# Kernel optimization log

Hardware: AMD Instinct MI355X
Metric: run time of the kernel (lower is better)

Reference implementation:

```python
import jax, jax.numpy as jnp
import numpy as np

HQ, HKV, HD = 32, 8, 64
ROPE_BASE = 10000.0


def _rope_cos_sin(L):
    # torchtune-style interleaved RoPE cache
    theta = 1.0 / (ROPE_BASE ** (jnp.arange(0, HD, 2, dtype=jnp.float32) / HD))  # [HD/2]
    ang = jnp.arange(L, dtype=jnp.float32)[:, None] * theta[None, :]             # [L, HD/2]
    return jnp.cos(ang)[None, :, None, :], jnp.sin(ang)[None, :, None, :]        # [1,L,1,HD/2]


def _apply_rope(t, cos, sin):
    # t: [B, L, H, HD]; pairs are interleaved along last dim
    x = t.reshape(t.shape[:-1] + (HD // 2, 2))
    x0, x1 = x[..., 0], x[..., 1]
    out = jnp.stack([x0 * cos - x1 * sin, x1 * cos + x0 * sin], axis=-1)
    return out.reshape(t.shape)


def setup_inputs() -> dict:
    key = jax.random.key(0)
    k1, k2, k3 = jax.random.split(key, 3)
    B, L, D = 2, 2048, 2048
    x = jax.random.normal(k1, (B, L, D), dtype=jnp.float32)
    w_qkv = jax.random.normal(k2, ((HQ + 2 * HKV) * HD, D), dtype=jnp.float32) * 0.02
    w_o = jax.random.normal(k3, (D, D), dtype=jnp.float32) * 0.02
    return {"x": x, "w_qkv": w_qkv, "w_o": w_o}


def reference(x, w_qkv, w_o):
    B, L, D = x.shape
    G = HQ // HKV  # q heads per kv head
    qkv = x @ w_qkv.T  # [B, L, (HQ+2*HKV)*HD]
    q = qkv[..., : HQ * HD].reshape(B, L, HQ, HD)
    k = qkv[..., HQ * HD : (HQ + HKV) * HD].reshape(B, L, HKV, HD)
    v = qkv[..., (HQ + HKV) * HD :].reshape(B, L, HKV, HD)

    cos, sin = _rope_cos_sin(L)
    q = _apply_rope(q, cos, sin)
    k = _apply_rope(k, cos, sin)

    # GQA: q head h attends with kv head h // G
    q = q.transpose(0, 2, 1, 3).reshape(B, HKV, G, L, HD)
    k = k.transpose(0, 2, 1, 3)  # [B, HKV, L, HD]
    v = v.transpose(0, 2, 1, 3)

    scale = 1.0 / jnp.sqrt(jnp.float32(HD))
    scores = jnp.einsum('bhgqd,bhkd->bhgqk', q, k) * scale  # [B,HKV,G,L,L]
    causal = jnp.tril(jnp.ones((L, L), dtype=bool))
    scores = jnp.where(causal, scores, jnp.finfo(scores.dtype).min)
    attn = jax.nn.softmax(scores, axis=-1)
    y = jnp.einsum('bhgqk,bhkd->bhgqd', attn, v)            # [B,HKV,G,L,HD]
    y = y.reshape(B, HQ, L, HD).transpose(0, 2, 1, 3).reshape(B, L, D)
    return y @ w_o.T
```

## Files before the change

### kernel.cpp

```cpp
#include <hip/hip_runtime.h>

typedef __attribute__((ext_vector_type(8))) short bf16x8;
typedef __attribute__((ext_vector_type(4))) float f32x4;

__device__ __forceinline__ float bf2f(unsigned short u) {
  unsigned int x = ((unsigned int)u) << 16;
  float f; __builtin_memcpy(&f, &x, 4); return f;
}
__device__ __forceinline__ unsigned short f2bf(float f) {
  unsigned int x; __builtin_memcpy(&x, &f, 4);
  unsigned int lsb = (x >> 16) & 1u;
  x += 0x7fffu + lsb;
  return (unsigned short)(x >> 16);
}
__device__ __forceinline__ unsigned short f2bf_trunc(float f) {
  unsigned int x; __builtin_memcpy(&x, &f, 4);
  return (unsigned short)(x >> 16);
}
__device__ __forceinline__ float exp2_raw(float x) {
  float r;
  asm("v_exp_f32 %0, %1" : "=v"(r) : "v"(x));
  return r;
}
__device__ __forceinline__ void gload16(const unsigned short* g, unsigned short* l) {
  __builtin_amdgcn_global_load_lds(
      (const __attribute__((address_space(1))) unsigned int*)g,
      (__attribute__((address_space(3))) unsigned int*)l, 16, 0, 0);
}

__global__ __launch_bounds__(256) void cvt3(const float* __restrict__ x,
                                            const float* __restrict__ wq,
                                            const float* __restrict__ wo,
                                            unsigned short* __restrict__ xb,
                                            unsigned short* __restrict__ wqb,
                                            unsigned short* __restrict__ wob) {
  const int N0 = 1048576, N1 = 786432, N2 = 524288;
  for (int i = blockIdx.x * 256 + threadIdx.x; i < N0 + N1 + N2;
       i += (int)(gridDim.x * 256)) {
    const float* in; unsigned short* out; int j;
    if (i < N0)            { in = x;  out = xb;  j = i; }
    else if (i < N0 + N1)  { in = wq; out = wqb; j = i - N0; }
    else                   { in = wo; out = wob; j = i - N0 - N1; }
    const float4* p = (const float4*)(in + (size_t)j * 8);
    float4 a = p[0], b = p[1];
    union { bf16x8 v; unsigned short u[8]; } o;
    o.u[0] = f2bf(a.x); o.u[1] = f2bf(a.y); o.u[2] = f2bf(a.z); o.u[3] = f2bf(a.w);
    o.u[4] = f2bf(b.x); o.u[5] = f2bf(b.y); o.u[6] = f2bf(b.z); o.u[7] = f2bf(b.w);
    *(bf16x8*)(out + (size_t)j * 8) = o.v;
  }
}

template <int F32OUT>
__global__ __launch_bounds__(256) void gemm_bt(const unsigned short* __restrict__ A,
                                               const unsigned short* __restrict__ B,
                                               void* __restrict__ Cp, int N) {
  __shared__ unsigned short sA[128 * 32];
  __shared__ unsigned short sB[128 * 32];
  const int t = threadIdx.x;
  const int lane = t & 63, w = t >> 6;
  const int wm = w >> 1, wn = w & 1;
  const int l16 = lane & 15, hi = lane >> 4;
  const int m0 = blockIdx.y * 128, n0 = blockIdx.x * 128;

  f32x4 zero = {0.f, 0.f, 0.f, 0.f};
  f32x4 acc[4][4];
#pragma unroll
  for (int mi = 0; mi < 4; ++mi)
#pragma unroll
    for (int ni = 0; ni < 4; ++ni) acc[mi][ni] = zero;

  const int srow = t >> 2;
  const int scol = (t & 3) * 8;
  const unsigned short* gA0 = A + (size_t)(m0 + srow) * 2048 + scol;
  const unsigned short* gB0 = B + (size_t)(n0 + srow) * 2048 + scol;

  int offA[4], offB[4];
#pragma unroll
  for (int i = 0; i < 4; ++i) {
    offA[i] = (wm * 64 + i * 16 + l16) * 32 + hi * 8;
    offB[i] = (wn * 64 + i * 16 + l16) * 32 + hi * 8;
  }

  for (int k0 = 0; k0 < 2048; k0 += 32) {
    __syncthreads();
    gload16(gA0 + k0, &sA[t * 8]);
    gload16(gA0 + (size_t)64 * 2048 + k0, &sA[2048 + t * 8]);
    gload16(gB0 + k0, &sB[t * 8]);
    gload16(gB0 + (size_t)64 * 2048 + k0, &sB[2048 + t * 8]);
    __syncthreads();
    bf16x8 af[4], bfr[4];
#pragma unroll
    for (int i = 0; i < 4; ++i) af[i] = *(const bf16x8*)&sA[offA[i]];
#pragma unroll
    for (int i = 0; i < 4; ++i) bfr[i] = *(const bf16x8*)&sB[offB[i]];
#pragma unroll
    for (int mi = 0; mi < 4; ++mi)
#pragma unroll
      for (int ni = 0; ni < 4; ++ni)
        acc[mi][ni] = __builtin_amdgcn_mfma_f32_16x16x32_bf16(af[mi], bfr[ni], acc[mi][ni], 0, 0, 0);
  }

  const int rowb = m0 + wm * 64 + hi * 4;
  const int colb = n0 + wn * 64 + l16;
#pragma unroll
  for (int mi = 0; mi < 4; ++mi)
#pragma unroll
    for (int ni = 0; ni < 4; ++ni)
#pragma unroll
      for (int r = 0; r < 4; ++r) {
        size_t idx = (size_t)(rowb + mi * 16 + r) * N + colb + ni * 16;
        if (F32OUT) ((float*)Cp)[idx] = acc[mi][ni][r];
        else        ((unsigned short*)Cp)[idx] = f2bf(acc[mi][ni][r]);
      }
}

__global__ __launch_bounds__(256) void prep(const unsigned short* __restrict__ qkv,
                                            unsigned short* __restrict__ q,
                                            unsigned short* __restrict__ k,
                                            unsigned short* __restrict__ vt) {
  __shared__ unsigned short sT[64 * 72];
  const int bid = blockIdx.x;
  if (bid < 640) {
    int tid = bid * 256 + threadIdx.x;
    int l = tid & 2047;
    int rest = tid >> 11;
    int b = rest & 1;
    int h = rest >> 1;
    const unsigned short* src = qkv + (size_t)(b * 2048 + l) * 3072 + h * 64;
    union { uint4 v[8]; unsigned short u[64]; } buf;
#pragma unroll
    for (int i = 0; i < 8; ++i) buf.v[i] = ((const uint4*)src)[i];
    const float sc = (h < 32) ? 0.125f * 1.44269504088896f : 1.0f;
#pragma unroll
    for (int j = 0; j < 32; ++j) {
      float fr = exp2f(-(float)j * 0.41524101186092033f);
      float ang = (float)l * fr;
      float sn, cs;
      sincosf(ang, &sn, &cs);
      float x0 = bf2f(buf.u[2 * j]), x1 = bf2f(buf.u[2 * j + 1]);
      float y0 = (x0 * cs - x1 * sn) * sc;
      float y1 = (x1 * cs + x0 * sn) * sc;
      buf.u[2 * j] = f2bf(y0);
      buf.u[2 * j + 1] = f2bf(y1);
    }
    unsigned short* dst = (h < 32) ? (q + ((size_t)(b * 32 + h) * 2048 + l) * 64)
                                   : (k + ((size_t)(b * 8 + h - 32) * 2048 + l) * 64);
#pragma unroll
    for (int i = 0; i < 8; ++i) ((uint4*)dst)[i] = buf.v[i];
  } else {
    const int bid2 = bid - 640;
    const int xb = bid2 & 31, bh = bid2 >> 5;
    const int t = threadIdx.x;
    const int b = bh >> 3, h = bh & 7;
    const int l0 = xb * 64;
    const int c = t & 7, i0 = t >> 3;
#pragma unroll
    for (int pp = 0; pp < 2; ++pp) {
      int i = i0 + pp * 32;
      const unsigned short* src =
          qkv + (size_t)(b * 2048 + l0 + i) * 3072 + 2560 + h * 64 + c * 8;
      union { bf16x8 v; unsigned short u[8]; } x;
      x.v = *(const bf16x8*)src;
#pragma unroll
      for (int e = 0; e < 8; ++e) sT[(c * 8 + e) * 72 + i] = x.u[e];
    }
    __syncthreads();
    const int d = t >> 2, ic = (t & 3) * 16;
    unsigned short* dst = vt + ((size_t)(b * 8 + h) * 64 + d) * 2048 + l0 + ic;
    *(bf16x8*)dst = *(const bf16x8*)&sT[d * 72 + ic];
    *(bf16x8*)(dst + 8) = *(const bf16x8*)&sT[d * 72 + ic + 8];
  }
}

__global__ __launch_bounds__(256) void attn(const unsigned short* __restrict__ Q,
                                            const unsigned short* __restrict__ K,
                                            const unsigned short* __restrict__ VT,
                                            unsigned short* __restrict__ Y) {
  __shared__ unsigned short sK[128 * 64];
  __shared__ unsigned short sV[64 * 128];
  __shared__ unsigned short sP[4][32 * 136];
  const int t = threadIdx.x, lane = t & 63, w = t >> 6;
  const int l16 = lane & 15, hi = lane >> 4;
  const int pi = blockIdx.y;
  const int bx = blockIdx.x;
  const int head = ((bx & 7) << 3) | (bx >> 3);
  const int b = head >> 5, hq = head & 31, hkv = hq >> 2;
  const unsigned short* kp = K + (size_t)(b * 8 + hkv) * 2048 * 64;
  const unsigned short* vp = VT + (size_t)(b * 8 + hkv) * 64 * 2048;
  unsigned short* sPw = sP[w];
  f32x4 zero = {0.f, 0.f, 0.f, 0.f};

#pragma unroll
  for (int phase = 0; phase < 2; ++phase) {
    const int qb = phase ? (15 - pi) : pi;
    const int q0 = qb * 128 + w * 32;
    const unsigned short* qp = Q + ((size_t)(b * 32 + hq) * 2048 + q0) * 64;

    bf16x8 qf[2][2];
#pragma unroll
    for (int mi = 0; mi < 2; ++mi)
#pragma unroll
      for (int ks = 0; ks < 2; ++ks)
        qf[mi][ks] = *(const bf16x8*)(qp + (size_t)(mi * 16 + l16) * 64 + ks * 32 + hi * 8);

    f32x4 o[2][4];
    float lsum[2][4];
#pragma unroll
    for (int mi = 0; mi < 2; ++mi) {
#pragma unroll
      for (int ni = 0; ni < 4; ++ni) o[mi][ni] = zero;
#pragma unroll
      for (int r = 0; r < 4; ++r) lsum[mi][r] = 0.f;
    }

    const int nt = qb + 1;
    for (int tt = 0; tt < nt; ++tt) {
      const int c0 = tt * 128;
      __syncthreads();
#pragma unroll
      for (int i = 0; i < 4; ++i) {
        int c = i * 256 + t;
        int row = c >> 3, cb = c & 7;
        gload16(kp + (size_t)(c0 + row) * 64 + ((cb ^ (row & 7)) * 8), &sK[c * 8]);
      }
#pragma unroll
      for (int i = 0; i < 4; ++i) {
        int c = i * 256 + t;
        int d = c >> 4, cb = c & 15;
        gload16(vp + (size_t)d * 2048 + c0 + ((cb ^ (d & 15)) * 8), &sV[c * 8]);
      }
      __syncthreads();

#pragma unroll
      for (int h = 0; h < 2; ++h) {
        const int c0h = c0 + h * 64;
        if (c0h > q0) break;
        f32x4 sc[2][4];
#pragma unroll
        for (int mi = 0; mi < 2; ++mi)
#pragma unroll
          for (int ni = 0; ni < 4; ++ni) sc[mi][ni] = zero;
#pragma unroll
        for (int ni = 0; ni < 4; ++ni) {
          const int krow = h * 64 + ni * 16 + l16;
          bf16x8 k0f = *(const bf16x8*)&sK[krow * 64 + ((hi ^ (l16 & 7)) * 8)];
          bf16x8 k1f = *(const bf16x8*)&sK[krow * 64 + (((4 + hi) ^ (l16 & 7)) * 8)];
#pragma unroll
          for (int mi = 0; mi < 2; ++mi) {
            sc[mi][ni] = __builtin_amdgcn_mfma_f32_16x16x32_bf16(qf[mi][0], k0f, sc[mi][ni], 0, 0, 0);
            sc[mi][ni] = __builtin_amdgcn_mfma_f32_16x16x32_bf16(qf[mi][1], k1f, sc[mi][ni], 0, 0, 0);
          }
        }
        if (c0h + 64 > q0) {
#pragma unroll
          for (int mi = 0; mi < 2; ++mi)
#pragma unroll
            for (int ni = 0; ni < 4; ++ni)
#pragma unroll
              for (int r = 0; r < 4; ++r) {
                int col = c0h + ni * 16 + l16;
                int row = q0 + mi * 16 + hi * 4 + r;
                if (col > row) sc[mi][ni][r] = -1e30f;
              }
        }
#pragma unroll
        for (int mi = 0; mi < 2; ++mi)
#pragma unroll
          for (int ni = 0; ni < 4; ++ni)
#pragma unroll
            for (int r = 0; r < 4; ++r) {
              float p = exp2_raw(sc[mi][ni][r]);
              lsum[mi][r] += p;
              sPw[(mi * 16 + hi * 4 + r) * 136 + h * 64 + ni * 16 + l16] = f2bf_trunc(p);
            }
      }
#pragma unroll
      for (int ks = 0; ks < 4; ++ks) {
        if (c0 + ks * 32 > q0) break;
        bf16x8 pa[2];
#pragma unroll
        for (int mi = 0; mi < 2; ++mi)
          pa[mi] = *(const bf16x8*)&sPw[(mi * 16 + l16) * 136 + ks * 32 + hi * 8];
#pragma unroll
        for (int ni = 0; ni < 4; ++ni) {
          const int d = ni * 16 + l16;
          bf16x8 vb = *(const bf16x8*)&sV[d * 128 + (((ks * 4 + hi) ^ l16) * 8)];
#pragma unroll
          for (int mi = 0; mi < 2; ++mi)
            o[mi][ni] = __builtin_amdgcn_mfma_f32_16x16x32_bf16(pa[mi], vb, o[mi][ni], 0, 0, 0);
        }
      }
    }
#pragma unroll
    for (int mi = 0; mi < 2; ++mi) {
#pragma unroll
      for (int msk = 1; msk <= 8; msk <<= 1)
#pragma unroll
        for (int r = 0; r < 4; ++r) lsum[mi][r] += __shfl_xor(lsum[mi][r], msk);
      float inv[4];
#pragma unroll
      for (int r = 0; r < 4; ++r) inv[r] = 1.f / lsum[mi][r];
#pragma unroll
      for (int ni = 0; ni < 4; ++ni)
#pragma unroll
        for (int r = 0; r < 4; ++r) {
          int row = q0 + mi * 16 + hi * 4 + r;
          Y[(size_t)(b * 2048 + row) * 2048 + hq * 64 + ni * 16 + l16] =
              f2bf(o[mi][ni][r] * inv[r]);
        }
    }
  }
}

extern "C" void kernel_launch(void* const* d_in, const int* in_sizes, int n_in,
                              void* d_out, int out_size, void* d_ws, size_t ws_size,
                              hipStream_t stream) {
  const float* x    = (const float*)d_in[0];
  const float* wqkv = (const float*)d_in[1];
  const float* wo   = (const float*)d_in[2];
  float* out = (float*)d_out;

  char* ws = (char*)d_ws;
  unsigned short* xb   = (unsigned short*)(ws);
  unsigned short* wqb  = (unsigned short*)(ws + 16777216);
  unsigned short* wob  = (unsigned short*)(ws + 29360128);
  unsigned short* qkvb = (unsigned short*)(ws + 37748736);
  unsigned short* qb   = (unsigned short*)(ws + 62914560);
  unsigned short* kb   = (unsigned short*)(ws + 79691776);
  unsigned short* vtb  = (unsigned short*)(ws + 83886080);
  unsigned short* yb = xb;

  cvt3<<<2048, 256, 0, stream>>>(x, wqkv, wo, xb, wqb, wob);
  gemm_bt<0><<<dim3(3072 / 128, 4096 / 128), 256, 0, stream>>>(xb, wqb, qkvb, 3072);
  prep<<<1152, 256, 0, stream>>>(qkvb, qb, kb, vtb);
  attn<<<dim3(64, 8), 256, 0, stream>>>(qb, kb, vtb, yb);
  gemm_bt<1><<<dim3(2048 / 128, 4096 / 128), 256, 0, stream>>>(yb, wob, out, 2048);
}
```

Before: 208.7 us.

## Double GEMM K-tile with XOR-swizzled LDS and compute softmax row sums via MFMA

The GEMM now stages 64-wide K tiles instead of 32, which halves the number of barrier-separated load phases. It also XOR-swizzles the shared-memory layout to avoid bank conflicts on the fragment reads. Separately, the attention kernel drops the scalar per-row probability accumulation and final cross-lane shuffle reduction. It instead multiplies the bf16 P tile by a ones vector with an extra MFMA per mi per ks step, so the row sum is taken from the same rounded bf16 values used for PV. This doubles GEMM LDS usage and adds MFMA work in attention in exchange for fewer VALU adds and shuffles.

```diff
diff --git a/kernel.cpp b/kernel.cpp
--- a/kernel.cpp
+++ b/kernel.cpp
@@ -54,8 +54,8 @@
 __global__ __launch_bounds__(256) void gemm_bt(const unsigned short* __restrict__ A,
                                                const unsigned short* __restrict__ B,
                                                void* __restrict__ Cp, int N) {
-  __shared__ unsigned short sA[128 * 32];
-  __shared__ unsigned short sB[128 * 32];
+  __shared__ unsigned short sA[128 * 64];
+  __shared__ unsigned short sB[128 * 64];
   const int t = threadIdx.x;
   const int lane = t & 63, w = t >> 6;
   const int wm = w >> 1, wn = w & 1;
@@ -69,35 +69,40 @@
 #pragma unroll
     for (int ni = 0; ni < 4; ++ni) acc[mi][ni] = zero;
 
-  const int srow = t >> 2;
-  const int scol = (t & 3) * 8;
-  const unsigned short* gA0 = A + (size_t)(m0 + srow) * 2048 + scol;
-  const unsigned short* gB0 = B + (size_t)(n0 + srow) * 2048 + scol;
-
-  int offA[4], offB[4];
-#pragma unroll
-  for (int i = 0; i < 4; ++i) {
-    offA[i] = (wm * 64 + i * 16 + l16) * 32 + hi * 8;
-    offB[i] = (wn * 64 + i * 16 + l16) * 32 + hi * 8;
-  }
-
-  for (int k0 = 0; k0 < 2048; k0 += 32) {
+  const unsigned short* gA = A + (size_t)m0 * 2048;
+  const unsigned short* gB = B + (size_t)n0 * 2048;
+
+  for (int k0 = 0; k0 < 2048; k0 += 64) {
     __syncthreads();
-    gload16(gA0 + k0, &sA[t * 8]);
-    gload16(gA0 + (size_t)64 * 2048 + k0, &sA[2048 + t * 8]);
-    gload16(gB0 + k0, &sB[t * 8]);
-    gload16(gB0 + (size_t)64 * 2048 + k0, &sB[2048 + t * 8]);
+#pragma unroll
+    for (int i = 0; i < 4; ++i) {
+      int c = i * 256 + t;
+      int row = c >> 3, cb = c & 7;
+      gload16(gA + (size_t)row * 2048 + k0 + ((cb ^ (row & 7)) * 8), &sA[c * 8]);
+    }
+#pragma unroll
+    for (int i = 0; i < 4; ++i) {
+      int c = i * 256 + t;
+      int row = c >> 3, cb = c & 7;
+      gload16(gB + (size_t)row * 2048 + k0 + ((cb ^ (row & 7)) * 8), &sB[c * 8]);
+    }
     __syncthreads();
-    bf16x8 af[4], bfr[4];
-#pragma unroll
-    for (int i = 0; i < 4; ++i) af[i] = *(const bf16x8*)&sA[offA[i]];
-#pragma unroll
-    for (int i = 0; i < 4; ++i) bfr[i] = *(const bf16x8*)&sB[offB[i]];
-#pragma unroll
-    for (int mi = 0; mi < 4; ++mi)
-#pragma unroll
-      for (int ni = 0; ni < 4; ++ni)
-        acc[mi][ni] = __builtin_amdgcn_mfma_f32_16x16x32_bf16(af[mi], bfr[ni], acc[mi][ni], 0, 0, 0);
+#pragma unroll
+    for (int kk = 0; kk < 2; ++kk) {
+      bf16x8 af[4], bfr[4];
+#pragma unroll
+      for (int i = 0; i < 4; ++i) {
+        int rowa = wm * 64 + i * 16 + l16;
+        af[i]  = *(const bf16x8*)&sA[rowa * 64 + (((kk * 4 + hi) ^ (l16 & 7)) * 8)];
+        int rowb = wn * 64 + i * 16 + l16;
+        bfr[i] = *(const bf16x8*)&sB[rowb * 64 + (((kk * 4 + hi) ^ (l16 & 7)) * 8)];
+      }
+#pragma unroll
+      for (int mi = 0; mi < 4; ++mi)
+#pragma unroll
+        for (int ni = 0; ni < 4; ++ni)
+          acc[mi][ni] = __builtin_amdgcn_mfma_f32_16x16x32_bf16(af[mi], bfr[ni], acc[mi][ni], 0, 0, 0);
+    }
   }
 
   const int rowb = m0 + wm * 64 + hi * 4;
@@ -189,6 +194,10 @@
   const unsigned short* vp = VT + (size_t)(b * 8 + hkv) * 64 * 2048;
   unsigned short* sPw = sP[w];
   f32x4 zero = {0.f, 0.f, 0.f, 0.f};
+  union { bf16x8 v; unsigned short u[8]; } ones_u;
+#pragma unroll
+  for (int j = 0; j < 8; ++j) ones_u.u[j] = 0x3F80;
+  const bf16x8 ones = ones_u.v;
 
 #pragma unroll
   for (int phase = 0; phase < 2; ++phase) {
@@ -204,13 +213,12 @@
         qf[mi][ks] = *(const bf16x8*)(qp + (size_t)(mi * 16 + l16) * 64 + ks * 32 + hi * 8);
 
     f32x4 o[2][4];
-    float lsum[2][4];
+    f32x4 os[2];
 #pragma unroll
     for (int mi = 0; mi < 2; ++mi) {
 #pragma unroll
       for (int ni = 0; ni < 4; ++ni) o[mi][ni] = zero;
-#pragma unroll
-      for (int r = 0; r < 4; ++r) lsum[mi][r] = 0.f;
+      os[mi] = zero;
     }
 
     const int nt = qb + 1;
@@ -270,7 +278,6 @@
 #pragma unroll
             for (int r = 0; r < 4; ++r) {
               float p = exp2_raw(sc[mi][ni][r]);
-              lsum[mi][r] += p;
               sPw[(mi * 16 + hi * 4 + r) * 136 + h * 64 + ni * 16 + l16] = f2bf_trunc(p);
             }
       }
@@ -279,8 +286,10 @@
         if (c0 + ks * 32 > q0) break;
         bf16x8 pa[2];
 #pragma unroll
-        for (int mi = 0; mi < 2; ++mi)
+        for (int mi = 0; mi < 2; ++mi) {
           pa[mi] = *(const bf16x8*)&sPw[(mi * 16 + l16) * 136 + ks * 32 + hi * 8];
+          os[mi] = __builtin_amdgcn_mfma_f32_16x16x32_bf16(pa[mi], ones, os[mi], 0, 0, 0);
+        }
 #pragma unroll
         for (int ni = 0; ni < 4; ++ni) {
           const int d = ni * 16 + l16;
@@ -293,13 +302,9 @@
     }
 #pragma unroll
     for (int mi = 0; mi < 2; ++mi) {
-#pragma unroll
-      for (int msk = 1; msk <= 8; msk <<= 1)
-#pragma unroll
-        for (int r = 0; r < 4; ++r) lsum[mi][r] += __shfl_xor(lsum[mi][r], msk);
       float inv[4];
 #pragma unroll
-      for (int r = 0; r < 4; ++r) inv[r] = 1.f / lsum[mi][r];
+      for (int r = 0; r < 4; ++r) inv[r] = 1.f / os[mi][r];
 #pragma unroll
       for (int ni = 0; ni < 4; ++ni)
 #pragma unroll
```

Measured after the change: 199.5 us. -4.4%, faster.
